# Kernel tuning notes

Measured on AMD Instinct MI355X. Metric: run time of the kernel, lower is better.

## Reference

```python
import jax, jax.numpy as jnp
import numpy as np

B, N, C, H = 4, 2048, 384, 6
D = C // H                       # head_dim = 64
HID = 4 * C                      # mlp hidden = 1536
SCALE = D ** -0.5
EPS = 1e-5                       # torch nn.LayerNorm default


def setup_inputs() -> dict:
    key = jax.random.key(0)
    ks = jax.random.split(key, 8)
    s = 0.02
    return {
        "x": jax.random.normal(ks[0], (B, N, C), jnp.float32),
        "ln1_g": jnp.ones((C,), jnp.float32),
        "ln1_b": jnp.zeros((C,), jnp.float32),
        "w_qkv": jax.random.normal(ks[1], (3 * C, C), jnp.float32) * s,
        "w_proj": jax.random.normal(ks[2], (C, C), jnp.float32) * s,
        "b_proj": jnp.zeros((C,), jnp.float32),
        "ln2_g": jnp.ones((C,), jnp.float32),
        "ln2_b": jnp.zeros((C,), jnp.float32),
        "w_fc1": jax.random.normal(ks[3], (HID, C), jnp.float32) * s,
        "b_fc1": jnp.zeros((HID,), jnp.float32),
        "w_fc2": jax.random.normal(ks[4], (C, HID), jnp.float32) * s,
        "b_fc2": jnp.zeros((C,), jnp.float32),
    }


def _layernorm(x, g, b):
    mu = jnp.mean(x, axis=-1, keepdims=True)
    var = jnp.mean(jnp.square(x - mu), axis=-1, keepdims=True)
    return (x - mu) * jax.lax.rsqrt(var + EPS) * g + b


def _bf16_round(x):
    # emulate the .bfloat16() cast after each residual (precision truncation)
    return x.astype(jnp.bfloat16).astype(jnp.float32)


def reference(x, ln1_g, ln1_b, w_qkv, w_proj, b_proj,
              ln2_g, ln2_b, w_fc1, b_fc1, w_fc2, b_fc2):
    # ---- attention branch (quant=False => HMQ ops are pass-through) ----
    h = _layernorm(x, ln1_g, ln1_b)                       # [B,N,C]
    qkv = jnp.einsum('bnc,oc->bno', h, w_qkv)             # [B,N,3C]
    qkv = qkv.reshape(B, N, 3, H, D).transpose(2, 0, 3, 1, 4)  # [3,B,H,N,D]
    q, k, v = qkv[0], qkv[1], qkv[2]
    attn = jnp.einsum('bhnd,bhmd->bhnm', q, k) * SCALE    # [B,H,N,N]
    attn = jax.nn.softmax(attn, axis=-1)
    o = jnp.einsum('bhnm,bhmd->bhnd', attn, v)            # [B,H,N,D]
    o = o.transpose(0, 2, 1, 3).reshape(B, N, C)
    o = jnp.einsum('bnc,oc->bno', o, w_proj) + b_proj
    x = _bf16_round(x + o)

    # ---- MLP branch ----
    h = _layernorm(x, ln2_g, ln2_b)
    h = jnp.einsum('bnc,hc->bnh', h, w_fc1) + b_fc1       # [B,N,HID]
    h = jax.nn.gelu(h, approximate=False)
    h = jnp.einsum('bnh,ch->bnc', h, w_fc2) + b_fc2       # [B,N,C]
    x = _bf16_round(x + h)
    return x
```

## Files before the change

kernel.cpp:

```cpp
#include <hip/hip_runtime.h>
#include <cstdint>
#include <cstddef>

#define DI __device__ __forceinline__

typedef __attribute__((ext_vector_type(8))) short short8;
typedef __attribute__((ext_vector_type(4))) float f32x4;
typedef unsigned int u32;
typedef unsigned short u16;

DI u16 rne_bf16(float f) {
  union { float f; u32 u; } v; v.f = f;
  u32 b = v.u;
  return (u16)((b + 0x7fffu + ((b >> 16) & 1u)) >> 16);
}
DI float bf2f(u16 h) {
  union { u32 u; float f; } v; v.u = ((u32)h) << 16;
  return v.f;
}
DI u32 cvtpk_bf16(float a, float b) {
  u32 r;
  asm("v_cvt_pk_bf16_f32 %0, %1, %2" : "=v"(r) : "v"(a), "v"(b));
  return r;
}

DI void gl2lds16(const void* g, void* l) {
  __builtin_amdgcn_global_load_lds(
      (const __attribute__((address_space(1))) u32*)g,
      (__attribute__((address_space(3))) u32*)l, 16, 0, 0);
}

DI void bar() {
  asm volatile("" ::: "memory");
  __builtin_amdgcn_s_barrier();
  asm volatile("" ::: "memory");
}

template<int ROWS, int NT>
DI void stage_swz(const u16* src, int ld, char* ldsb, int tid) {
  int wbase = tid & ~63;
  #pragma unroll
  for (int c = 0; c < (ROWS * 8) / NT; ++c) {
    int g = c * NT + tid;
    int row = g >> 3;
    int sgr = (g & 7) ^ (row & 7);
    gl2lds16(src + row * ld + sgr * 8, ldsb + (size_t)(c * NT + wbase) * 16);
  }
}

DI short8 lds_frag(const char* base, int row, int k0) {
  return *(const short8*)(base + row * 128 + ((k0 * 2) ^ ((row & 7) << 4)));
}

DI f32x4 mfma16(short8 a, short8 b, f32x4 c) {
  return __builtin_amdgcn_mfma_f32_16x16x32_bf16(a, b, c, 0, 0, 0);
}

__global__ __launch_bounds__(256) void cvt_w(
    const float* __restrict__ a, const float* __restrict__ b,
    const float* __restrict__ c, const float* __restrict__ d,
    u16* __restrict__ oa, u16* __restrict__ ob, u16* __restrict__ oc,
    u16* __restrict__ od) {
  int i = blockIdx.x * 256 + threadIdx.x;
  if (i < 442368) oa[i] = rne_bf16(a[i]);
  else if (i < 589824) ob[i - 442368] = rne_bf16(b[i - 442368]);
  else if (i < 1179648) oc[i - 589824] = rne_bf16(c[i - 589824]);
  else if (i < 1769472) od[i - 1179648] = rne_bf16(d[i - 1179648]);
}

template<int INBF>
__global__ __launch_bounds__(256) void ln_k(
    const void* __restrict__ xin, const float* __restrict__ gam,
    const float* __restrict__ bet, u16* __restrict__ out) {
  int row = blockIdx.x * 4 + (threadIdx.x >> 6);
  int lane = threadIdx.x & 63;
  float v[6];
  if (INBF) {
    const u16* x = (const u16*)xin + (size_t)row * 384 + lane * 6;
    #pragma unroll
    for (int j = 0; j < 6; ++j) v[j] = bf2f(x[j]);
  } else {
    const float* x = (const float*)xin + (size_t)row * 384 + lane * 6;
    #pragma unroll
    for (int j = 0; j < 6; ++j) v[j] = x[j];
  }
  float s = 0.f;
  #pragma unroll
  for (int j = 0; j < 6; ++j) s += v[j];
  #pragma unroll
  for (int d = 1; d < 64; d <<= 1) s += __shfl_xor(s, d);
  float mu = s * (1.f / 384.f);
  float q = 0.f;
  #pragma unroll
  for (int j = 0; j < 6; ++j) { float t = v[j] - mu; q += t * t; }
  #pragma unroll
  for (int d = 1; d < 64; d <<= 1) q += __shfl_xor(q, d);
  float rstd = rsqrtf(q * (1.f / 384.f) + 1e-5f);
  #pragma unroll
  for (int j = 0; j < 6; ++j) {
    int c = lane * 6 + j;
    out[(size_t)row * 384 + c] = rne_bf16((v[j] - mu) * rstd * gam[c] + bet[c]);
  }
}

struct EpiP {
  const float* bias;
  const float* residf;
  const u16* residb;
  u16* outb;
  float* outf;
  u16* q; u16* k; u16* v;
};

#define QSCALE 0.18033688011112042f

template<int EPI, int MT>
__global__ __launch_bounds__(256) void gemm_bt(
    const u16* __restrict__ A, const u16* __restrict__ W, int K, int bnN,
    EpiP p) {
  constexpr int ABUF = MT * 128;
  constexpr int NC = (MT == 128) ? 4 : 2;
  __shared__ char lds[2 * (ABUF + 16384)];
  int tid = threadIdx.x, lane = tid & 63, wid = tid >> 6;
  int wr = (MT == 128) ? (wid >> 1) * 64 : 0;
  int wcb = (MT == 128) ? (wid & 1) * 64 : wid * 32;
  int fr = lane & 15, k8 = lane >> 4;
  int orig = blockIdx.x;
  int cpx = (int)gridDim.x >> 3;
  int wg = (orig & 7) * cpx + (orig >> 3);
  int bm = wg / bnN, bn = wg - bm * bnN;
  const u16* Ab = A + (size_t)bm * MT * K;
  const u16* Wb = W + (size_t)bn * 128 * K;

  stage_swz<MT, 256>(Ab, K, lds, tid);
  stage_swz<128, 256>(Wb, K, lds + ABUF, tid);

  f32x4 zz = {0.f, 0.f, 0.f, 0.f};
  f32x4 acc[4][NC];
  #pragma unroll
  for (int mr = 0; mr < 4; ++mr)
    #pragma unroll
    for (int nc = 0; nc < NC; ++nc) acc[mr][nc] = zz;

  asm volatile("s_waitcnt vmcnt(0)" ::: "memory");
  __syncthreads();

  int KT = K >> 6;
  for (int t = 0; t < KT; ++t) {
    char* base = lds + (size_t)(t & 1) * (ABUF + 16384);
    if (t + 1 < KT) {
      char* nb = lds + (size_t)((t + 1) & 1) * (ABUF + 16384);
      stage_swz<MT, 256>(Ab + (t + 1) * 64, K, nb, tid);
      stage_swz<128, 256>(Wb + (t + 1) * 64, K, nb + ABUF, tid);
    }
    #pragma unroll
    for (int ks = 0; ks < 2; ++ks) {
      int k0 = ks * 32 + k8 * 8;
      short8 av[4], bv[NC];
      #pragma unroll
      for (int mr = 0; mr < 4; ++mr) av[mr] = lds_frag(base, wr + mr * 16 + fr, k0);
      #pragma unroll
      for (int nc = 0; nc < NC; ++nc) bv[nc] = lds_frag(base + ABUF, wcb + nc * 16 + fr, k0);
      __builtin_amdgcn_s_setprio(1);
      #pragma unroll
      for (int mr = 0; mr < 4; ++mr)
        #pragma unroll
        for (int nc = 0; nc < NC; ++nc)
          acc[mr][nc] = mfma16(av[mr], bv[nc], acc[mr][nc]);
      __builtin_amdgcn_s_setprio(0);
    }
    asm volatile("s_waitcnt vmcnt(0)" ::: "memory");
    __syncthreads();
  }

  #pragma unroll
  for (int mr = 0; mr < 4; ++mr)
    #pragma unroll
    for (int nc = 0; nc < NC; ++nc)
      #pragma unroll
      for (int r = 0; r < 4; ++r) {
        int m = bm * MT + wr + mr * 16 + k8 * 4 + r;
        int o = bn * 128 + wcb + nc * 16 + fr;
        float val = acc[mr][nc][r];
        if constexpr (EPI == 0) {
          int tq = o / 384;
          int rem = o - tq * 384;
          int hh = rem >> 6, d = rem & 63;
          int b = m >> 11, n = m & 2047;
          float sv = (tq == 0) ? val * QSCALE : val;
          u16 bvs = rne_bf16(sv);
          size_t qk = (((size_t)(b * 6 + hh)) * 2048 + n) * 64 + d;
          if (tq == 0) p.q[qk] = bvs;
          else if (tq == 1) p.k[qk] = bvs;
          else p.v[qk] = bvs;
        } else if constexpr (EPI == 1) {
          size_t idx = (size_t)m * 384 + o;
          float r2 = p.residf[idx] + val + p.bias[o];
          p.outb[idx] = rne_bf16(r2);
        } else if constexpr (EPI == 2) {
          size_t idx = (size_t)m * 1536 + o;
          float z = val + p.bias[o];
          float gl = 0.5f * z * (1.f + erff(z * 0.70710678118654752f));
          p.outb[idx] = rne_bf16(gl);
        } else {
          size_t idx = (size_t)m * 384 + o;
          float r2 = bf2f(p.residb[idx]) + val + p.bias[o];
          p.outf[idx] = bf2f(rne_bf16(r2));
        }
      }
}

__global__ __launch_bounds__(256) void vtr_k(
    const u16* __restrict__ v, u16* __restrict__ vt) {
  __shared__ u16 t[64 * 72];
  int tid = threadIdx.x;
  int n0 = blockIdx.x * 64, bh = blockIdx.y;
  const u16* src = v + ((size_t)bh * 2048 + n0) * 64;
  #pragma unroll
  for (int it = 0; it < 2; ++it) {
    int row = it * 32 + (tid >> 3), c8 = tid & 7;
    *(short8*)&t[row * 72 + c8 * 8] = *(const short8*)(src + row * 64 + c8 * 8);
  }
  __syncthreads();
  int d = tid & 63, c = tid >> 6;
  u16 o[16];
  #pragma unroll
  for (int j = 0; j < 16; ++j) o[j] = t[(c * 16 + j) * 72 + d];
  u16* dst = vt + ((size_t)bh * 64 + d) * 2048 + n0 + c * 16;
  *(short8*)dst = *(short8*)&o[0];
  *(short8*)(dst + 8) = *(short8*)&o[8];
}

__global__ __launch_bounds__(512, 6) void attn_k(
    const u16* __restrict__ Qg, const u16* __restrict__ Kg,
    const u16* __restrict__ Vg, float* __restrict__ Op, float* __restrict__ lp) {
  __shared__ char lds[51712];
  int tid = threadIdx.x, lane = tid & 63, wid = tid >> 6;
  int fr = lane & 15, k8 = lane >> 4;
  int qt = blockIdx.x, bh = blockIdx.y, z = blockIdx.z;
  const u16* Qb = Qg + (size_t)bh * 2048 * 64;
  const u16* Kb = Kg + ((size_t)bh * 2048 + z * 1024) * 64;
  const u16* Vb = Vg + (size_t)bh * 64 * 2048 + z * 1024;
  int qr0 = qt * 128 + wid * 16;

  short8 qf[2];
  #pragma unroll
  for (int ks = 0; ks < 2; ++ks)
    qf[ks] = *(const short8*)(Qb + (size_t)(qr0 + fr) * 64 + ks * 32 + k8 * 8);

  f32x4 zz = {0.f, 0.f, 0.f, 0.f};
  f32x4 oacc[4];
  float lrun[4];
  #pragma unroll
  for (int nc = 0; nc < 4; ++nc) oacc[nc] = zz;
  #pragma unroll
  for (int r = 0; r < 4; ++r) lrun[r] = 0.f;
  char* P = lds + 32768 + wid * 2368;
  char* Pw = P + (k8 * 4) * 148 + fr * 2;
  char* Pr = P + fr * 148;

  #define STAGE(t)                                                             \
    stage_swz<64, 512>(Kb + (size_t)(t) * 4096, 64, lds + ((t) & 1) * 8192, tid); \
    stage_swz<64, 512>(Vb + (t) * 64, 2048, lds + 16384 + ((t) & 1) * 8192, tid);

  STAGE(0);
  asm volatile("s_waitcnt vmcnt(0)" ::: "memory");
  bar();

  for (int t = 0; t < 16; ++t) {
    if (t + 1 < 16) { STAGE(t + 1); }
    char* kbase = lds + (t & 1) * 8192;
    char* vbase = lds + 16384 + (t & 1) * 8192;
    f32x4 s[4];
    #pragma unroll
    for (int nc = 0; nc < 4; ++nc) s[nc] = zz;
    #pragma unroll
    for (int ks = 0; ks < 2; ++ks) {
      int k0 = ks * 32 + k8 * 8;
      short8 kf[4];
      #pragma unroll
      for (int nc = 0; nc < 4; ++nc) kf[nc] = lds_frag(kbase, nc * 16 + fr, k0);
      __builtin_amdgcn_s_setprio(1);
      #pragma unroll
      for (int nc = 0; nc < 4; ++nc) s[nc] = mfma16(qf[ks], kf[nc], s[nc]);
      __builtin_amdgcn_s_setprio(0);
    }
    #pragma unroll
    for (int nc = 0; nc < 4; ++nc)
      #pragma unroll
      for (int rp = 0; rp < 2; ++rp) {
        float p0 = exp2f(s[nc][2 * rp]);
        float p1 = exp2f(s[nc][2 * rp + 1]);
        lrun[2 * rp] += p0;
        lrun[2 * rp + 1] += p1;
        u32 w = cvtpk_bf16(p0, p1);
        *(u16*)(Pw + (2 * rp) * 148 + nc * 32) = (u16)w;
        *(u16*)(Pw + (2 * rp + 1) * 148 + nc * 32) = (u16)(w >> 16);
      }
    #pragma unroll
    for (int ks = 0; ks < 2; ++ks) {
      int k0 = ks * 32 + k8 * 8;
      short8 pa = *(const short8*)(Pr + k0 * 2);
      short8 vf[4];
      #pragma unroll
      for (int nc = 0; nc < 4; ++nc) vf[nc] = lds_frag(vbase, nc * 16 + fr, k0);
      __builtin_amdgcn_s_setprio(1);
      #pragma unroll
      for (int nc = 0; nc < 4; ++nc) oacc[nc] = mfma16(pa, vf[nc], oacc[nc]);
      __builtin_amdgcn_s_setprio(0);
    }
    asm volatile("s_waitcnt vmcnt(0)" ::: "memory");
    if (t < 15) bar();
  }
  #undef STAGE

  #pragma unroll
  for (int r = 0; r < 4; ++r) {
    float t2 = lrun[r];
    #pragma unroll
    for (int dd = 1; dd < 16; dd <<= 1) t2 += __shfl_xor(t2, dd);
    lrun[r] = t2;
  }
  size_t rowb = (size_t)z * 49152 + (size_t)bh * 2048;
  #pragma unroll
  for (int nc = 0; nc < 4; ++nc)
    #pragma unroll
    for (int r = 0; r < 4; ++r) {
      int qrow = qr0 + k8 * 4 + r;
      Op[(rowb + qrow) * 64 + nc * 16 + fr] = oacc[nc][r];
    }
  if (fr == 0)
    #pragma unroll
    for (int r = 0; r < 4; ++r)
      lp[rowb + qr0 + k8 * 4 + r] = lrun[r];
}

__global__ __launch_bounds__(256) void attn_merge(
    const float* __restrict__ Op, const float* __restrict__ lp,
    u16* __restrict__ ao) {
  int row = blockIdx.x * 4 + (threadIdx.x >> 6);
  int d = threadIdx.x & 63;
  float l = lp[row] + lp[49152 + row];
  float v = (Op[(size_t)row * 64 + d] + Op[(size_t)(49152 + row) * 64 + d]) / l;
  int bh = row >> 11, n = row & 2047;
  int b = bh / 6, hh = bh - b * 6;
  ao[((size_t)(b * 2048 + n)) * 384 + hh * 64 + d] = rne_bf16(v);
}

extern "C" void kernel_launch(void* const* d_in, const int* in_sizes, int n_in,
                              void* d_out, int out_size, void* d_ws, size_t ws_size,
                              hipStream_t stream) {
  const float* x     = (const float*)d_in[0];
  const float* ln1g  = (const float*)d_in[1];
  const float* ln1b  = (const float*)d_in[2];
  const float* wqkv  = (const float*)d_in[3];
  const float* wproj = (const float*)d_in[4];
  const float* bproj = (const float*)d_in[5];
  const float* ln2g  = (const float*)d_in[6];
  const float* ln2b  = (const float*)d_in[7];
  const float* wfc1  = (const float*)d_in[8];
  const float* bfc1  = (const float*)d_in[9];
  const float* wfc2  = (const float*)d_in[10];
  const float* bfc2  = (const float*)d_in[11];
  float* out = (float*)d_out;

  char* w = (char*)d_ws;
  u16* h1     = (u16*)w; w += 6291456;
  u16* x2     = (u16*)w; w += 6291456;
  u16* h2     = (u16*)w; w += 6291456;
  u16* qb     = (u16*)w; w += 6291456;
  u16* kb     = (u16*)w; w += 6291456;
  u16* vtb    = (u16*)w; w += 6291456;
  u16* ao     = (u16*)w; w += 6291456;
  u16* act    = (u16*)w; w += 25165824;
  u16* wqkvb  = (u16*)w; w += 884736;
  u16* wprojb = (u16*)w; w += 294912;
  u16* wfc1b  = (u16*)w; w += 1179648;
  u16* wfc2b  = (u16*)w; w += 1179648;

  u16* v_nat   = h2;
  float* Opart = (float*)act;
  float* lpart = (float*)h2;

  cvt_w<<<6912, 256, 0, stream>>>(wqkv, wproj, wfc1, wfc2, wqkvb, wprojb, wfc1b, wfc2b);
  ln_k<0><<<2048, 256, 0, stream>>>(x, ln1g, ln1b, h1);
  {
    EpiP p{}; p.q = qb; p.k = kb; p.v = v_nat;
    gemm_bt<0, 64><<<1152, 256, 0, stream>>>(h1, wqkvb, 384, 9, p);
  }
  vtr_k<<<dim3(32, 24), 256, 0, stream>>>(v_nat, vtb);
  attn_k<<<dim3(16, 24, 2), 512, 0, stream>>>(qb, kb, vtb, Opart, lpart);
  attn_merge<<<12288, 256, 0, stream>>>(Opart, lpart, ao);
  {
    EpiP p{}; p.bias = bproj; p.residf = x; p.outb = x2;
    gemm_bt<1, 64><<<384, 256, 0, stream>>>(ao, wprojb, 384, 3, p);
  }
  ln_k<1><<<2048, 256, 0, stream>>>(x2, ln2g, ln2b, h2);
  {
    EpiP p{}; p.bias = bfc1; p.outb = act;
    gemm_bt<2, 128><<<768, 256, 0, stream>>>(h2, wfc1b, 384, 12, p);
  }
  {
    EpiP p{}; p.bias = bfc2; p.residb = x2; p.outf = out;
    gemm_bt<3, 64><<<384, 256, 0, stream>>>(act, wfc2b, 1536, 3, p);
  }
}
```

Before: 247.4 us.

## Give each attention warp two query row tiles and compute row sums via MFMA

The attention kernel now runs 256 threads per block, with each wave handling 32 query rows (two 16-row tiles). Each K/V fragment read from LDS is therefore reused across twice as many MFMAs. The softmax denominator is now accumulated with an extra MFMA against a vector of bf16 ones, which replaces the scalar adds and the cross-lane shuffle reduction. The V-transpose kernel switches to 32-bit LDS reads with a padded stride, and LayerNorm loads become lane-strided so accesses coalesce. The cost is more registers per wave, fewer waves per block, and the occupancy hint has been dropped.

New measurement: 241.6 us. -2.3%, faster.

```diff
diff --git a/kernel.cpp b/kernel.cpp
--- a/kernel.cpp
+++ b/kernel.cpp
@@ -76,13 +76,13 @@
   int lane = threadIdx.x & 63;
   float v[6];
   if (INBF) {
-    const u16* x = (const u16*)xin + (size_t)row * 384 + lane * 6;
-    #pragma unroll
-    for (int j = 0; j < 6; ++j) v[j] = bf2f(x[j]);
+    const u16* x = (const u16*)xin + (size_t)row * 384 + lane;
+    #pragma unroll
+    for (int j = 0; j < 6; ++j) v[j] = bf2f(x[j * 64]);
   } else {
-    const float* x = (const float*)xin + (size_t)row * 384 + lane * 6;
-    #pragma unroll
-    for (int j = 0; j < 6; ++j) v[j] = x[j];
+    const float* x = (const float*)xin + (size_t)row * 384 + lane;
+    #pragma unroll
+    for (int j = 0; j < 6; ++j) v[j] = x[j * 64];
   }
   float s = 0.f;
   #pragma unroll
@@ -98,7 +98,7 @@
   float rstd = rsqrtf(q * (1.f / 384.f) + 1e-5f);
   #pragma unroll
   for (int j = 0; j < 6; ++j) {
-    int c = lane * 6 + j;
+    int c = j * 64 + lane;
     out[(size_t)row * 384 + c] = rne_bf16((v[j] - mu) * rstd * gam[c] + bet[c]);
   }
 }
@@ -212,26 +212,30 @@
 
 __global__ __launch_bounds__(256) void vtr_k(
     const u16* __restrict__ v, u16* __restrict__ vt) {
-  __shared__ u16 t[64 * 72];
+  __shared__ u16 t[64 * 74];
   int tid = threadIdx.x;
   int n0 = blockIdx.x * 64, bh = blockIdx.y;
   const u16* src = v + ((size_t)bh * 2048 + n0) * 64;
   #pragma unroll
   for (int it = 0; it < 2; ++it) {
     int row = it * 32 + (tid >> 3), c8 = tid & 7;
-    *(short8*)&t[row * 72 + c8 * 8] = *(const short8*)(src + row * 64 + c8 * 8);
+    *(short8*)&t[row * 74 + c8 * 8] = *(const short8*)(src + row * 64 + c8 * 8);
   }
   __syncthreads();
-  int d = tid & 63, c = tid >> 6;
-  u16 o[16];
-  #pragma unroll
-  for (int j = 0; j < 16; ++j) o[j] = t[(c * 16 + j) * 72 + d];
-  u16* dst = vt + ((size_t)bh * 64 + d) * 2048 + n0 + c * 16;
-  *(short8*)dst = *(short8*)&o[0];
-  *(short8*)(dst + 8) = *(short8*)&o[8];
-}
-
-__global__ __launch_bounds__(512, 6) void attn_k(
+  int dp = tid >> 3;
+  int ng = tid & 7;
+  u16 lo[8], hi[8];
+  #pragma unroll
+  for (int j = 0; j < 8; ++j) {
+    u32 a = *(const u32*)&t[(ng * 8 + j) * 74 + dp * 2];
+    lo[j] = (u16)a; hi[j] = (u16)(a >> 16);
+  }
+  u16* dst = vt + ((size_t)bh * 64 + 2 * dp) * 2048 + n0 + ng * 8;
+  *(short8*)dst = *(short8*)&lo[0];
+  *(short8*)(dst + 2048) = *(short8*)&hi[0];
+}
+
+__global__ __launch_bounds__(256) void attn_k(
     const u16* __restrict__ Qg, const u16* __restrict__ Kg,
     const u16* __restrict__ Vg, float* __restrict__ Op, float* __restrict__ lp) {
   __shared__ char lds[51712];
@@ -241,27 +245,32 @@
   const u16* Qb = Qg + (size_t)bh * 2048 * 64;
   const u16* Kb = Kg + ((size_t)bh * 2048 + z * 1024) * 64;
   const u16* Vb = Vg + (size_t)bh * 64 * 2048 + z * 1024;
-  int qr0 = qt * 128 + wid * 16;
-
-  short8 qf[2];
-  #pragma unroll
-  for (int ks = 0; ks < 2; ++ks)
-    qf[ks] = *(const short8*)(Qb + (size_t)(qr0 + fr) * 64 + ks * 32 + k8 * 8);
+  int qr0 = qt * 128 + wid * 32;
+
+  short8 qf[2][2];
+  #pragma unroll
+  for (int mr = 0; mr < 2; ++mr)
+    #pragma unroll
+    for (int ks = 0; ks < 2; ++ks)
+      qf[mr][ks] = *(const short8*)(Qb + (size_t)(qr0 + mr * 16 + fr) * 64 + ks * 32 + k8 * 8);
+
+  short8 ones;
+  #pragma unroll
+  for (int i = 0; i < 8; ++i) ones[i] = (short)0x3F80;
 
   f32x4 zz = {0.f, 0.f, 0.f, 0.f};
-  f32x4 oacc[4];
-  float lrun[4];
-  #pragma unroll
-  for (int nc = 0; nc < 4; ++nc) oacc[nc] = zz;
-  #pragma unroll
-  for (int r = 0; r < 4; ++r) lrun[r] = 0.f;
-  char* P = lds + 32768 + wid * 2368;
-  char* Pw = P + (k8 * 4) * 148 + fr * 2;
-  char* Pr = P + fr * 148;
-
-  #define STAGE(t)                                                             \
-    stage_swz<64, 512>(Kb + (size_t)(t) * 4096, 64, lds + ((t) & 1) * 8192, tid); \
-    stage_swz<64, 512>(Vb + (t) * 64, 2048, lds + 16384 + ((t) & 1) * 8192, tid);
+  f32x4 oacc[2][4], lacc[2];
+  #pragma unroll
+  for (int mr = 0; mr < 2; ++mr) {
+    #pragma unroll
+    for (int nc = 0; nc < 4; ++nc) oacc[mr][nc] = zz;
+    lacc[mr] = zz;
+  }
+  char* P = lds + 32768 + wid * 4736;
+
+  #define STAGE(t)                                                              \
+    stage_swz<64, 256>(Kb + (size_t)(t) * 4096, 64, lds + ((t) & 1) * 8192, tid); \
+    stage_swz<64, 256>(Vb + (t) * 64, 2048, lds + 16384 + ((t) & 1) * 8192, tid);
 
   STAGE(0);
   asm volatile("s_waitcnt vmcnt(0)" ::: "memory");
@@ -271,9 +280,11 @@
     if (t + 1 < 16) { STAGE(t + 1); }
     char* kbase = lds + (t & 1) * 8192;
     char* vbase = lds + 16384 + (t & 1) * 8192;
-    f32x4 s[4];
-    #pragma unroll
-    for (int nc = 0; nc < 4; ++nc) s[nc] = zz;
+    f32x4 s[2][4];
+    #pragma unroll
+    for (int mr = 0; mr < 2; ++mr)
+      #pragma unroll
+      for (int nc = 0; nc < 4; ++nc) s[mr][nc] = zz;
     #pragma unroll
     for (int ks = 0; ks < 2; ++ks) {
       int k0 = ks * 32 + k8 * 8;
@@ -282,31 +293,42 @@
       for (int nc = 0; nc < 4; ++nc) kf[nc] = lds_frag(kbase, nc * 16 + fr, k0);
       __builtin_amdgcn_s_setprio(1);
       #pragma unroll
-      for (int nc = 0; nc < 4; ++nc) s[nc] = mfma16(qf[ks], kf[nc], s[nc]);
+      for (int mr = 0; mr < 2; ++mr)
+        #pragma unroll
+        for (int nc = 0; nc < 4; ++nc)
+          s[mr][nc] = mfma16(qf[mr][ks], kf[nc], s[mr][nc]);
       __builtin_amdgcn_s_setprio(0);
     }
     #pragma unroll
-    for (int nc = 0; nc < 4; ++nc)
-      #pragma unroll
-      for (int rp = 0; rp < 2; ++rp) {
-        float p0 = exp2f(s[nc][2 * rp]);
-        float p1 = exp2f(s[nc][2 * rp + 1]);
-        lrun[2 * rp] += p0;
-        lrun[2 * rp + 1] += p1;
-        u32 w = cvtpk_bf16(p0, p1);
-        *(u16*)(Pw + (2 * rp) * 148 + nc * 32) = (u16)w;
-        *(u16*)(Pw + (2 * rp + 1) * 148 + nc * 32) = (u16)(w >> 16);
-      }
+    for (int mr = 0; mr < 2; ++mr)
+      #pragma unroll
+      for (int nc = 0; nc < 4; ++nc)
+        #pragma unroll
+        for (int rp = 0; rp < 2; ++rp) {
+          float p0 = exp2f(s[mr][nc][2 * rp]);
+          float p1 = exp2f(s[mr][nc][2 * rp + 1]);
+          u32 w = cvtpk_bf16(p0, p1);
+          char* base = P + (mr * 16 + k8 * 4 + 2 * rp) * 148 + (nc * 16 + fr) * 2;
+          *(u16*)base = (u16)w;
+          *(u16*)(base + 148) = (u16)(w >> 16);
+        }
     #pragma unroll
     for (int ks = 0; ks < 2; ++ks) {
       int k0 = ks * 32 + k8 * 8;
-      short8 pa = *(const short8*)(Pr + k0 * 2);
-      short8 vf[4];
+      short8 pa[2], vf[4];
+      #pragma unroll
+      for (int mr = 0; mr < 2; ++mr)
+        pa[mr] = *(const short8*)(P + (mr * 16 + fr) * 148 + k0 * 2);
       #pragma unroll
       for (int nc = 0; nc < 4; ++nc) vf[nc] = lds_frag(vbase, nc * 16 + fr, k0);
       __builtin_amdgcn_s_setprio(1);
       #pragma unroll
-      for (int nc = 0; nc < 4; ++nc) oacc[nc] = mfma16(pa, vf[nc], oacc[nc]);
+      for (int mr = 0; mr < 2; ++mr) {
+        #pragma unroll
+        for (int nc = 0; nc < 4; ++nc)
+          oacc[mr][nc] = mfma16(pa[mr], vf[nc], oacc[mr][nc]);
+        lacc[mr] = mfma16(pa[mr], ones, lacc[mr]);
+      }
       __builtin_amdgcn_s_setprio(0);
     }
     asm volatile("s_waitcnt vmcnt(0)" ::: "memory");
@@ -314,25 +336,22 @@
   }
   #undef STAGE
 
-  #pragma unroll
-  for (int r = 0; r < 4; ++r) {
-    float t2 = lrun[r];
-    #pragma unroll
-    for (int dd = 1; dd < 16; dd <<= 1) t2 += __shfl_xor(t2, dd);
-    lrun[r] = t2;
-  }
   size_t rowb = (size_t)z * 49152 + (size_t)bh * 2048;
   #pragma unroll
-  for (int nc = 0; nc < 4; ++nc)
-    #pragma unroll
-    for (int r = 0; r < 4; ++r) {
-      int qrow = qr0 + k8 * 4 + r;
-      Op[(rowb + qrow) * 64 + nc * 16 + fr] = oacc[nc][r];
-    }
+  for (int mr = 0; mr < 2; ++mr)
+    #pragma unroll
+    for (int nc = 0; nc < 4; ++nc)
+      #pragma unroll
+      for (int r = 0; r < 4; ++r) {
+        int qrow = qr0 + mr * 16 + k8 * 4 + r;
+        Op[(rowb + qrow) * 64 + nc * 16 + fr] = oacc[mr][nc][r];
+      }
   if (fr == 0)
     #pragma unroll
-    for (int r = 0; r < 4; ++r)
-      lp[rowb + qr0 + k8 * 4 + r] = lrun[r];
+    for (int mr = 0; mr < 2; ++mr)
+      #pragma unroll
+      for (int r = 0; r < 4; ++r)
+        lp[rowb + qr0 + mr * 16 + k8 * 4 + r] = lacc[mr][r];
 }
 
 __global__ __launch_bounds__(256) void attn_merge(
@@ -389,7 +408,7 @@
     gemm_bt<0, 64><<<1152, 256, 0, stream>>>(h1, wqkvb, 384, 9, p);
   }
   vtr_k<<<dim3(32, 24), 256, 0, stream>>>(v_nat, vtb);
-  attn_k<<<dim3(16, 24, 2), 512, 0, stream>>>(qb, kb, vtb, Opart, lpart);
+  attn_k<<<dim3(16, 24, 2), 256, 0, stream>>>(qb, kb, vtb, Opart, lpart);
   attn_merge<<<12288, 256, 0, stream>>>(Opart, lpart, ao);
   {
     EpiP p{}; p.bias = bproj; p.residf = x; p.outb = x2;
```
